# Kernel optimization log

Measured on AMD Instinct MI355X. Metric: run time of the kernel, lower is better.

## Reference

```python
import jax, jax.numpy as jnp
import numpy as np

EPS = 1e-7   # keras backend epsilon used by K.ctc_batch_cost
NEG = -1e30  # log-space -inf surrogate (fp32-safe)


def ctc_batch_cost(labels, y_pred):
    """Faithful jax port of tf.keras.backend.ctc_batch_cost with
    input_length = T and label_length = L for every batch row (as in CTCLayer).
    labels: [B, L] int, values in [0, C-2]; y_pred: [B, T, C] probabilities.
    Blank index = C-1. Returns loss [B, 1]."""
    B, T, C = y_pred.shape
    L = labels.shape[1]
    S = 2 * L + 1
    blank = C - 1
    log_probs = jnp.log(y_pred + EPS)  # [B, T, C]

    # extended label sequence: blank, l1, blank, l2, ..., blank  -> [B, S]
    ext = jnp.full((B, S), blank, dtype=jnp.int32)
    ext = ext.at[:, 1::2].set(labels.astype(jnp.int32))

    # per-frame log-probs of extended labels: [B, T, S]
    lp = jnp.take_along_axis(log_probs, jnp.broadcast_to(ext[:, None, :], (B, T, S)), axis=2)

    # skip transition allowed at s iff ext[s] != blank and ext[s] != ext[s-2]
    skip = jnp.concatenate(
        [jnp.zeros((B, 2), dtype=bool),
         (ext[:, 2:] != ext[:, :-2]) & (ext[:, 2:] != blank)], axis=1)  # [B, S]

    # init alpha at t=0
    alpha0 = jnp.full((B, S), NEG, dtype=log_probs.dtype)
    alpha0 = alpha0.at[:, 0].set(lp[:, 0, 0]).at[:, 1].set(lp[:, 0, 1])

    def step(alpha, lp_t):
        a1 = alpha
        a2 = jnp.pad(alpha[:, :-1], ((0, 0), (1, 0)), constant_values=NEG)
        a3 = jnp.where(skip, jnp.pad(alpha[:, :-2], ((0, 0), (2, 0)), constant_values=NEG), NEG)
        new = jnp.logaddexp(jnp.logaddexp(a1, a2), a3) + lp_t
        return new, None

    # scan over time steps 1..T-1; lp time-major [T-1, B, S]
    alpha, _ = jax.lax.scan(step, alpha0, jnp.swapaxes(lp, 0, 1)[1:])

    loss = -jnp.logaddexp(alpha[:, S - 1], alpha[:, S - 2])  # [B]
    return loss[:, None]  # [B, 1], matching ctc_batch_cost


def setup_inputs() -> dict:
    key = jax.random.key(0)
    k1, k2 = jax.random.split(key)
    y_pred = jax.random.uniform(k1, (256, 512, 512), dtype=jnp.float32)  # probs in (0,1)
    y_true = jax.random.randint(k2, (256, 128), 0, 511)  # labels, blank=511 excluded
    return {"y_true": y_true, "y_pred": y_pred}


def reference(y_true, y_pred):
    return ctc_batch_cost(y_true, y_pred)
```

## Files before the change

### kernel.cpp

```cpp
#include <hip/hip_runtime.h>

namespace {

constexpr int   kT = 512, kC = 512, kL = 128, kBlank = 511;
constexpr int   kCH  = 16;
constexpr int   kNCH = kT / kCH;
constexpr float kEps = 1e-7f, kLn2 = 0.6931471805599453f;

typedef float __attribute__((address_space(1))) f32g;
typedef float __attribute__((address_space(3))) f32l;

__device__ __forceinline__ void glds16(const float* g, float* l) {
    __builtin_amdgcn_global_load_lds((const f32g*)g, (f32l*)l, 16, 0, 0);
}
__device__ __forceinline__ float rlane(float x, int l) {
    return __int_as_float(__builtin_amdgcn_readlane(__float_as_int(x), l));
}
__device__ __forceinline__ float bperm(int a, float x) {
    return __int_as_float(__builtin_amdgcn_ds_bpermute(a, __float_as_int(x)));
}
__device__ __forceinline__ float LOG2(float x) { return __builtin_amdgcn_logf(x); }

__device__ __forceinline__ void barrier_raw() {
    asm volatile("" ::: "memory");
    __builtin_amdgcn_s_barrier();
    asm volatile("" ::: "memory");
}

__global__ __launch_bounds__(128, 1) void ctc_fwd_kernel(
        const int* __restrict__ labels,
        const float* __restrict__ y_pred,
        float* __restrict__ out) {
    __shared__ __align__(16) float buf[3][kCH][kC];

    const int tid  = (int)threadIdx.x;
    const int lane = tid & 63;
    const int wv   = tid >> 6;
    const int b    = (int)blockIdx.x;
    const float* yp  = y_pred + (size_t)b * kT * kC;
    const int*   lab = labels + b * kL;

    int   cls1 = kBlank, cls3 = kBlank;
    float skp1 = 0.f, skp3 = 0.f;
    if (wv == 0) {
        cls1 = lab[2 * lane];
        cls3 = lab[2 * lane + 1];
        skp1 = (lane >= 1 && lab[2 * lane] != lab[2 * lane - 1]) ? 1.f : 0.f;
        skp3 = (lab[2 * lane + 1] != lab[2 * lane]) ? 1.f : 0.f;
    }
    const int addr1 = (lane - 1) << 2;

    float g_rb[kCH], g_r1[kCH], g_r3[kCH];

    float (*bC)[kC] = buf[0];
    float (*bN)[kC] = buf[1];
    float (*bP)[kC] = buf[2];

    if (wv == 1) {
        for (int ch = 0; ch < 3; ++ch) {
            for (int r = 0; r < kCH; ++r) {
                const float* row = yp + (size_t)(ch * kCH + r) * kC;
                glds16(row + lane * 4,       &buf[ch][r][0]);
                glds16(row + 256 + lane * 4, &buf[ch][r][256]);
            }
        }
        asm volatile("s_waitcnt vmcnt(32)" ::: "memory");
    }
    barrier_raw();
    if (wv == 0) {
#pragma unroll
        for (int r = 0; r < kCH; ++r) {
            g_rb[r] = bC[r][kBlank];
            g_r1[r] = bC[r][cls1];
            g_r3[r] = bC[r][cls3];
        }
        asm volatile("s_waitcnt lgkmcnt(0)" ::: "memory");
    }
    barrier_raw();

    float a0 = 0.f, a1 = 0.f, a2 = 0.f, a3 = 0.f, a256 = 0.f, etot = 0.f;
    float inj = (lane == 0) ? 1.f : 0.f;

    for (int c = 0; c < kNCH; ++c) {
        if (wv == 1) {
            if (c + 3 < kNCH) {
                for (int r = 0; r < kCH; ++r) {
                    const float* row = yp + (size_t)((c + 3) * kCH + r) * kC;
                    glds16(row + lane * 4,       &bC[r][0]);
                    glds16(row + 256 + lane * 4, &bC[r][256]);
                }
                asm volatile("s_waitcnt vmcnt(32)" ::: "memory");
            } else if (c == kNCH - 3) {
                asm volatile("s_waitcnt vmcnt(0)" ::: "memory");
            }
        } else {
#pragma unroll
            for (int r = 0; r < kCH; ++r) {
                const float pb = g_rb[r] + kEps;
                const float p1 = g_r1[r] + kEps;
                const float p3 = g_r3[r] + kEps;
                float sh3 = bperm(addr1, a3);
                sh3 = (lane == 0) ? 0.f : sh3;
                const float a255 = rlane(a3, 63);
                const float b0 = (a0 + sh3 + inj) * pb;
                const float b1 = (a1 + a0 + skp1 * sh3 + inj) * p1;
                const float b2 = (a2 + a1) * pb;
                const float b3 = (a3 + a2 + skp3 * a1) * p3;
                a256 = (a256 + a255) * pb;
                a0 = b0; a1 = b1; a2 = b2; a3 = b3;
                inj = 0.f;
            }
            if (c & 1) {
                float m = fmaxf(fmaxf(a0, a1), fmaxf(a2, a3));
#pragma unroll
                for (int i = 1; i < 64; i <<= 1) m = fmaxf(m, __shfl_xor(m, i));
                m = fmaxf(m, a256);
                const int ex = (__float_as_int(m) >> 23) & 0xFF;
                if (ex > 1) {
                    const float sc = __int_as_float((254 - ex) << 23);
                    a0 *= sc; a1 *= sc; a2 *= sc; a3 *= sc; a256 *= sc;
                    etot += (float)(ex - 127);
                }
            }
            if (c + 1 < kNCH) {
#pragma unroll
                for (int r = 0; r < kCH; ++r) {
                    g_rb[r] = bN[r][kBlank];
                    g_r1[r] = bN[r][cls1];
                    g_r3[r] = bN[r][cls3];
                }
            }
            asm volatile("s_waitcnt lgkmcnt(0)" ::: "memory");
        }
        barrier_raw();
        float (*tmp)[kC] = bC; bC = bN; bN = bP; bP = tmp;
    }

    if (wv == 0) {
        const float a255 = rlane(a3, 63);
        const float s    = a255 + a256;
        const float loss = -kLn2 * (LOG2(s) + etot);
        if (lane == 0) out[b] = loss;
    }
}

}

extern "C" void kernel_launch(void* const* d_in, const int* in_sizes, int n_in,
                              void* d_out, int out_size, void* d_ws, size_t ws_size,
                              hipStream_t stream) {
    const int*   labels = (const int*)d_in[0];
    const float* y_pred = (const float*)d_in[1];
    float*       out    = (float*)d_out;
    (void)in_sizes; (void)n_in; (void)d_ws; (void)ws_size;
    hipLaunchKernelGGL(ctc_fwd_kernel, dim3(out_size), dim3(128), 0, stream,
                       labels, y_pred, out);
}
```

Measured before the change: 54.28 us.

## Merge producer and consumer waves into one wave with double-buffered LDS

Replaces the two-wave producer/consumer scheme (one wave issuing global-to-LDS loads, one running the CTC recurrence, synchronised by barriers) with a single wave that issues the async loads itself and double-buffers LDS. Per-chunk label gathers become inline-asm ds_read batches with immediate offsets, followed by explicit waits and scheduling barriers. This removes per-chunk workgroup barriers and the triple-buffer rotation. In exchange, load issue now sits on the serial recurrence path and the prefetch depth drops from three chunks to two.

Result: slower. 59.84 us (+10.2%).

```diff
diff --git a/kernel.cpp b/kernel.cpp
--- a/kernel.cpp
+++ b/kernel.cpp
@@ -21,122 +21,127 @@
 }
 __device__ __forceinline__ float LOG2(float x) { return __builtin_amdgcn_logf(x); }
 
-__device__ __forceinline__ void barrier_raw() {
-    asm volatile("" ::: "memory");
-    __builtin_amdgcn_s_barrier();
-    asm volatile("" ::: "memory");
-}
+#define GATHER16(dst_, addr_)                                                 \
+    asm volatile("ds_read_b32 %0, %16 offset:0\n\t"                           \
+                 "ds_read_b32 %1, %16 offset:2048\n\t"                        \
+                 "ds_read_b32 %2, %16 offset:4096\n\t"                        \
+                 "ds_read_b32 %3, %16 offset:6144\n\t"                        \
+                 "ds_read_b32 %4, %16 offset:8192\n\t"                        \
+                 "ds_read_b32 %5, %16 offset:10240\n\t"                       \
+                 "ds_read_b32 %6, %16 offset:12288\n\t"                       \
+                 "ds_read_b32 %7, %16 offset:14336\n\t"                       \
+                 "ds_read_b32 %8, %16 offset:16384\n\t"                       \
+                 "ds_read_b32 %9, %16 offset:18432\n\t"                       \
+                 "ds_read_b32 %10, %16 offset:20480\n\t"                      \
+                 "ds_read_b32 %11, %16 offset:22528\n\t"                      \
+                 "ds_read_b32 %12, %16 offset:24576\n\t"                      \
+                 "ds_read_b32 %13, %16 offset:26624\n\t"                      \
+                 "ds_read_b32 %14, %16 offset:28672\n\t"                      \
+                 "ds_read_b32 %15, %16 offset:30720"                          \
+                 : "=&v"(dst_[0]), "=&v"(dst_[1]), "=&v"(dst_[2]),            \
+                   "=&v"(dst_[3]), "=&v"(dst_[4]), "=&v"(dst_[5]),            \
+                   "=&v"(dst_[6]), "=&v"(dst_[7]), "=&v"(dst_[8]),            \
+                   "=&v"(dst_[9]), "=&v"(dst_[10]), "=&v"(dst_[11]),          \
+                   "=&v"(dst_[12]), "=&v"(dst_[13]), "=&v"(dst_[14]),         \
+                   "=&v"(dst_[15])                                            \
+                 : "v"(addr_))
 
-__global__ __launch_bounds__(128, 1) void ctc_fwd_kernel(
+__global__ __launch_bounds__(64, 1) void ctc_fwd_kernel(
         const int* __restrict__ labels,
         const float* __restrict__ y_pred,
         float* __restrict__ out) {
-    __shared__ __align__(16) float buf[3][kCH][kC];
+    __shared__ __align__(16) float buf[2][kCH][kC];
 
-    const int tid  = (int)threadIdx.x;
-    const int lane = tid & 63;
-    const int wv   = tid >> 6;
+    const int lane = (int)threadIdx.x;
     const int b    = (int)blockIdx.x;
     const float* yp  = y_pred + (size_t)b * kT * kC;
     const int*   lab = labels + b * kL;
 
-    int   cls1 = kBlank, cls3 = kBlank;
-    float skp1 = 0.f, skp3 = 0.f;
-    if (wv == 0) {
-        cls1 = lab[2 * lane];
-        cls3 = lab[2 * lane + 1];
-        skp1 = (lane >= 1 && lab[2 * lane] != lab[2 * lane - 1]) ? 1.f : 0.f;
-        skp3 = (lab[2 * lane + 1] != lab[2 * lane]) ? 1.f : 0.f;
-    }
+    const int l0  = lab[2 * lane];
+    const int l1v = lab[2 * lane + 1];
+    const int lm  = (lane >= 1) ? lab[2 * lane - 1] : 0;
+    const int cls1 = l0, cls3 = l1v;
+    const float skp1 = (lane >= 1 && l0 != lm) ? 1.f : 0.f;
+    const float skp3 = (l1v != l0) ? 1.f : 0.f;
     const int addr1 = (lane - 1) << 2;
 
+    const unsigned aBb = (unsigned)(uintptr_t)&buf[0][0][kBlank];
+    const unsigned aB1 = (unsigned)(uintptr_t)&buf[0][0][cls1];
+    const unsigned aB3 = (unsigned)(uintptr_t)&buf[0][0][cls3];
+
+    asm volatile("s_waitcnt vmcnt(0)" ::: "memory");
+    __builtin_amdgcn_sched_barrier(0);
+
+    for (int ch = 0; ch < 2; ++ch)
+        for (int r = 0; r < kCH; ++r) {
+            const float* row = yp + (size_t)(ch * kCH + r) * kC;
+            glds16(row + lane * 4,       &buf[ch][r][0]);
+            glds16(row + 256 + lane * 4, &buf[ch][r][256]);
+        }
+    asm volatile("s_waitcnt vmcnt(32)" ::: "memory");
+
     float g_rb[kCH], g_r1[kCH], g_r3[kCH];
-
-    float (*bC)[kC] = buf[0];
-    float (*bN)[kC] = buf[1];
-    float (*bP)[kC] = buf[2];
-
-    if (wv == 1) {
-        for (int ch = 0; ch < 3; ++ch) {
-            for (int r = 0; r < kCH; ++r) {
-                const float* row = yp + (size_t)(ch * kCH + r) * kC;
-                glds16(row + lane * 4,       &buf[ch][r][0]);
-                glds16(row + 256 + lane * 4, &buf[ch][r][256]);
-            }
-        }
-        asm volatile("s_waitcnt vmcnt(32)" ::: "memory");
-    }
-    barrier_raw();
-    if (wv == 0) {
-#pragma unroll
-        for (int r = 0; r < kCH; ++r) {
-            g_rb[r] = bC[r][kBlank];
-            g_r1[r] = bC[r][cls1];
-            g_r3[r] = bC[r][cls3];
-        }
-        asm volatile("s_waitcnt lgkmcnt(0)" ::: "memory");
-    }
-    barrier_raw();
+    GATHER16(g_rb, aBb);
+    GATHER16(g_r1, aB1);
+    GATHER16(g_r3, aB3);
+    asm volatile("s_waitcnt lgkmcnt(0)" ::: "memory");
+    __builtin_amdgcn_sched_barrier(0);
 
     float a0 = 0.f, a1 = 0.f, a2 = 0.f, a3 = 0.f, a256 = 0.f, etot = 0.f;
     float inj = (lane == 0) ? 1.f : 0.f;
 
     for (int c = 0; c < kNCH; ++c) {
-        if (wv == 1) {
-            if (c + 3 < kNCH) {
-                for (int r = 0; r < kCH; ++r) {
-                    const float* row = yp + (size_t)((c + 3) * kCH + r) * kC;
-                    glds16(row + lane * 4,       &bC[r][0]);
-                    glds16(row + 256 + lane * 4, &bC[r][256]);
-                }
+        if (c + 2 < kNCH) {
+            float (*bS)[kC] = buf[c & 1];
+            for (int r = 0; r < kCH; ++r) {
+                const float* row = yp + (size_t)((c + 2) * kCH + r) * kC;
+                glds16(row + lane * 4,       &bS[r][0]);
+                glds16(row + 256 + lane * 4, &bS[r][256]);
+            }
+        }
+#pragma unroll
+        for (int r = 0; r < kCH; ++r) {
+            const float pb = g_rb[r] + kEps;
+            const float p1 = g_r1[r] + kEps;
+            const float p3 = g_r3[r] + kEps;
+            float sh3 = bperm(addr1, a3);
+            sh3 = (lane == 0) ? 0.f : sh3;
+            const float a255 = rlane(a3, 63);
+            const float b0 = (a0 + sh3 + inj) * pb;
+            const float b1 = (a1 + a0 + skp1 * sh3 + inj) * p1;
+            const float b2 = (a2 + a1) * pb;
+            const float b3 = (a3 + a2 + skp3 * a1) * p3;
+            a256 = (a256 + a255) * pb;
+            a0 = b0; a1 = b1; a2 = b2; a3 = b3;
+            inj = 0.f;
+        }
+        if (c & 1) {
+            float m = fmaxf(fmaxf(a0, a1), fmaxf(a2, a3));
+#pragma unroll
+            for (int i = 1; i < 64; i <<= 1) m = fmaxf(m, __shfl_xor(m, i));
+            m = fmaxf(m, a256);
+            const int ex = (__float_as_int(m) >> 23) & 0xFF;
+            if (ex > 1) {
+                const float sc = __int_as_float((254 - ex) << 23);
+                a0 *= sc; a1 *= sc; a2 *= sc; a3 *= sc; a256 *= sc;
+                etot += (float)(ex - 127);
+            }
+        }
+        if (c + 1 < kNCH) {
+            if (c + 2 < kNCH)
                 asm volatile("s_waitcnt vmcnt(32)" ::: "memory");
-            } else if (c == kNCH - 3) {
+            else
                 asm volatile("s_waitcnt vmcnt(0)" ::: "memory");
-            }
-        } else {
-#pragma unroll
-            for (int r = 0; r < kCH; ++r) {
-                const float pb = g_rb[r] + kEps;
-                const float p1 = g_r1[r] + kEps;
-                const float p3 = g_r3[r] + kEps;
-                float sh3 = bperm(addr1, a3);
-                sh3 = (lane == 0) ? 0.f : sh3;
-                const float a255 = rlane(a3, 63);
-                const float b0 = (a0 + sh3 + inj) * pb;
-                const float b1 = (a1 + a0 + skp1 * sh3 + inj) * p1;
-                const float b2 = (a2 + a1) * pb;
-                const float b3 = (a3 + a2 + skp3 * a1) * p3;
-                a256 = (a256 + a255) * pb;
-                a0 = b0; a1 = b1; a2 = b2; a3 = b3;
-                inj = 0.f;
-            }
-            if (c & 1) {
-                float m = fmaxf(fmaxf(a0, a1), fmaxf(a2, a3));
-#pragma unroll
-                for (int i = 1; i < 64; i <<= 1) m = fmaxf(m, __shfl_xor(m, i));
-                m = fmaxf(m, a256);
-                const int ex = (__float_as_int(m) >> 23) & 0xFF;
-                if (ex > 1) {
-                    const float sc = __int_as_float((254 - ex) << 23);
-                    a0 *= sc; a1 *= sc; a2 *= sc; a3 *= sc; a256 *= sc;
-                    etot += (float)(ex - 127);
-                }
-            }
-            if (c + 1 < kNCH) {
-#pragma unroll
-                for (int r = 0; r < kCH; ++r) {
-                    g_rb[r] = bN[r][kBlank];
-                    g_r1[r] = bN[r][cls1];
-                    g_r3[r] = bN[r][cls3];
-                }
-            }
+            const unsigned off = (unsigned)(((c + 1) & 1) * (kCH * kC * 4));
+            GATHER16(g_rb, aBb + off);
+            GATHER16(g_r1, aB1 + off);
+            GATHER16(g_r3, aB3 + off);
             asm volatile("s_waitcnt lgkmcnt(0)" ::: "memory");
+            __builtin_amdgcn_sched_barrier(0);
         }
-        barrier_raw();
-        float (*tmp)[kC] = bC; bC = bN; bN = bP; bP = tmp;
     }
 
-    if (wv == 0) {
+    {
         const float a255 = rlane(a3, 63);
         const float s    = a255 + a256;
         const float loss = -kLn2 * (LOG2(s) + etot);
@@ -153,6 +158,6 @@
     const float* y_pred = (const float*)d_in[1];
     float*       out    = (float*)d_out;
     (void)in_sizes; (void)n_in; (void)d_ws; (void)ws_size;
-    hipLaunchKernelGGL(ctc_fwd_kernel, dim3(out_size), dim3(128), 0, stream,
+    hipLaunchKernelGGL(ctc_fwd_kernel, dim3(out_size), dim3(64), 0, stream,
                        labels, y_pred, out);
 }
```
